# Optimization experiments

Hardware: AMD Instinct MI355X
Metric: run time of the kernel (lower is better)

The kernel has to match this reference:

```python
import jax, jax.numpy as jnp
import numpy as np

N_STATE = 64   # S4 state size N
L_MAX = 4096   # sequence length
H = 256        # number of SSM channels (d_model)
BATCH = 16


def _green_roots(Lambda, P, B, C, step, L):
    """Frequency-domain S4 kernel at the L roots of unity (Q = P, DPLR).
    Lambda,P,B,C: complex[N]; step: scalar. Returns complex[L]."""
    Omega = jnp.exp(-2j * jnp.pi * (jnp.arange(L) / L))          # (L,)
    g = (2.0 / step) * ((1.0 - Omega) / (1.0 + Omega))           # (L,)
    c = 2.0 / (1.0 + Omega)                                      # (L,)
    # four Cauchy numerators stacked: k00,k01,k10,k11
    vs = jnp.stack([C.conj() * B, C.conj() * P,
                    P.conj() * B, P.conj() * P])                 # (4,N)
    denom = g[:, None] - Lambda[None, :]                         # (L,N)
    k = jnp.einsum('kn,ln->kl', vs, 1.0 / denom)                 # (4,L)
    k00, k01, k10, k11 = k
    return c * (k00 - k01 * (1.0 / (1.0 + k11)) * k10)           # (L,)


def _kernel_freq(Lambda_re, Lambda_im, P_re, P_im, B_re, B_im,
                 C_re, C_im, log_step, L):
    Lambda = (Lambda_re + 1j * Lambda_im).astype(jnp.complex64)  # (H,N)
    P = (P_re + 1j * P_im).astype(jnp.complex64)
    Bm = (B_re + 1j * B_im).astype(jnp.complex64)
    Cm = (C_re + 1j * C_im).astype(jnp.complex64)
    step = jnp.exp(log_step)                                     # (H,)
    f = lambda lam, p, b, c, s: _green_roots(lam, p, b, c, s, L)
    return jax.vmap(f)(Lambda, P, Bm, Cm, step)                  # (H,L)


def setup_inputs() -> dict:
    key = jax.random.key(0)
    ks = jax.random.split(key, 10)
    u = jax.random.normal(ks[0], (BATCH, H, L_MAX), dtype=jnp.float32)
    # stable continuous-time poles: negative real part, spread imag parts
    Lambda_re = -0.5 * jnp.ones((H, N_STATE), jnp.float32) \
        - jax.random.uniform(ks[1], (H, N_STATE), dtype=jnp.float32)
    Lambda_im = jnp.pi * jax.random.normal(ks[2], (H, N_STATE), dtype=jnp.float32) * N_STATE / 8
    scale = 1.0 / np.sqrt(N_STATE)
    P_re = scale * jax.random.normal(ks[3], (H, N_STATE), dtype=jnp.float32)
    P_im = scale * jax.random.normal(ks[4], (H, N_STATE), dtype=jnp.float32)
    B_re = scale * jax.random.normal(ks[5], (H, N_STATE), dtype=jnp.float32)
    B_im = scale * jax.random.normal(ks[6], (H, N_STATE), dtype=jnp.float32)
    C_re = scale * jax.random.normal(ks[7], (H, N_STATE), dtype=jnp.float32)
    C_im = scale * jax.random.normal(ks[8], (H, N_STATE), dtype=jnp.float32)
    # log-uniform step in [1e-3, 1e-1] (log_step_initializer)
    log_step = (jax.random.uniform(ks[9], (H,), dtype=jnp.float32)
                * (np.log(0.1) - np.log(0.001)) + np.log(0.001)).astype(jnp.float32)
    return {"u": u, "Lambda_re": Lambda_re, "Lambda_im": Lambda_im,
            "P_re": P_re, "P_im": P_im, "B_re": B_re, "B_im": B_im,
            "C_re": C_re, "C_im": C_im, "log_step": log_step}


def reference(u, Lambda_re, Lambda_im, P_re, P_im, B_re, B_im,
              C_re, C_im, log_step):
    L = u.shape[-1]
    Kf = _kernel_freq(Lambda_re, Lambda_im, P_re, P_im, B_re, B_im,
                      C_re, C_im, log_step, L)                   # (H,L) complex
    # circular_convolution_complex, batched over (BATCH,H)
    ud = jnp.fft.fft(u, axis=-1)                                  # (B,H,L)
    y = jnp.fft.ifft(ud * Kf[None, :, :], n=L, axis=-1)
    return y.real.astype(jnp.float32)                             # (B,H,L)
```

## Files before the change

### kernel.cpp

```cpp
#include <hip/hip_runtime.h>
#include <math.h>

#define NSTATE 64
#define LEN    4096
#define NH     256
#define NB     16

__device__ float2 g_knat[NH * LEN];
__device__ float2 g_ksym[NH * LEN];
__device__ float4 g_pA[NH * NSTATE];
__device__ float4 g_pB[NH * NSTATE];
__device__ float2 g_pC[NH * NSTATE];

__device__ __forceinline__ int rev8_12(int p) {
  return ((p & 7) << 9) | (((p >> 3) & 7) << 6) | (((p >> 6) & 7) << 3) | (p >> 9);
}

__device__ __forceinline__ float2 cadd(float2 a, float2 b){ return make_float2(a.x+b.x, a.y+b.y); }
__device__ __forceinline__ float2 csub(float2 a, float2 b){ return make_float2(a.x-b.x, a.y-b.y); }
__device__ __forceinline__ float2 cmul(float2 a, float2 b){ return make_float2(a.x*b.x - a.y*b.y, a.x*b.y + a.y*b.x); }
__device__ __forceinline__ float2 mulnegi(float2 a){ return make_float2(a.y, -a.x); }
__device__ __forceinline__ float2 mulposi(float2 a){ return make_float2(-a.y, a.x); }

#define RSQ2 0.70710678118654752f

__device__ __forceinline__ void bfly8_fwd(float2 v[8]) {
  float2 a0 = cadd(v[0], v[4]), b0 = csub(v[0], v[4]);
  float2 a1 = cadd(v[1], v[5]), d1 = csub(v[1], v[5]);
  float2 a2 = cadd(v[2], v[6]), d2 = csub(v[2], v[6]);
  float2 a3 = cadd(v[3], v[7]), d3 = csub(v[3], v[7]);
  float2 b1 = make_float2(RSQ2 * (d1.x + d1.y), RSQ2 * (d1.y - d1.x));
  float2 b2 = mulnegi(d2);
  float2 b3 = make_float2(RSQ2 * (d3.y - d3.x), -RSQ2 * (d3.x + d3.y));
  float2 u0 = cadd(a0, a2), u1 = csub(a0, a2), u2 = cadd(a1, a3), u3 = csub(a1, a3);
  v[0] = cadd(u0, u2);
  v[2] = cadd(u1, mulnegi(u3));
  v[4] = csub(u0, u2);
  v[6] = cadd(u1, mulposi(u3));
  float2 w0 = cadd(b0, b2), w1 = csub(b0, b2), w2 = cadd(b1, b3), w3 = csub(b1, b3);
  v[1] = cadd(w0, w2);
  v[3] = cadd(w1, mulnegi(w3));
  v[5] = csub(w0, w2);
  v[7] = cadd(w1, mulposi(w3));
}

__device__ __forceinline__ void bfly8_inv(float2 v[8]) {
  float2 a0 = cadd(v[0], v[4]), b0 = csub(v[0], v[4]);
  float2 a1 = cadd(v[1], v[5]), d1 = csub(v[1], v[5]);
  float2 a2 = cadd(v[2], v[6]), d2 = csub(v[2], v[6]);
  float2 a3 = cadd(v[3], v[7]), d3 = csub(v[3], v[7]);
  float2 b1 = make_float2(RSQ2 * (d1.x - d1.y), RSQ2 * (d1.x + d1.y));
  float2 b2 = mulposi(d2);
  float2 b3 = make_float2(-RSQ2 * (d3.x + d3.y), RSQ2 * (d3.x - d3.y));
  float2 u0 = cadd(a0, a2), u1 = csub(a0, a2), u2 = cadd(a1, a3), u3 = csub(a1, a3);
  v[0] = cadd(u0, u2);
  v[2] = cadd(u1, mulposi(u3));
  v[4] = csub(u0, u2);
  v[6] = cadd(u1, mulnegi(u3));
  float2 w0 = cadd(b0, b2), w1 = csub(b0, b2), w2 = cadd(b1, b3), w3 = csub(b1, b3);
  v[1] = cadd(w0, w2);
  v[3] = cadd(w1, mulposi(w3));
  v[5] = csub(w0, w2);
  v[7] = cadd(w1, mulnegi(w3));
}

__device__ __forceinline__ void twiddle7(float2 v[8], float wr, float wi) {
  float2 w1 = make_float2(wr, wi);
  float2 w2 = cmul(w1, w1);
  float2 w3 = cmul(w2, w1);
  float2 w4 = cmul(w2, w2);
  float2 w5 = cmul(w3, w2);
  float2 w6 = cmul(w3, w3);
  float2 w7 = cmul(w4, w3);
  v[1] = cmul(v[1], w1); v[2] = cmul(v[2], w2); v[3] = cmul(v[3], w3);
  v[4] = cmul(v[4], w4); v[5] = cmul(v[5], w5); v[6] = cmul(v[6], w6);
  v[7] = cmul(v[7], w7);
}

__global__ __launch_bounds__(256) void s4_prep(
    const float* __restrict__ Lre, const float* __restrict__ Lim,
    const float* __restrict__ Pre, const float* __restrict__ Pim,
    const float* __restrict__ Bre, const float* __restrict__ Bim,
    const float* __restrict__ Cre, const float* __restrict__ Cim)
{
  int idx = blockIdx.x * 256 + threadIdx.x;
  if (idx >= NH * NSTATE) return;
  float lr = Lre[idx], li = Lim[idx];
  float pr = Pre[idx], pi = Pim[idx];
  float br = Bre[idx], bi = Bim[idx];
  float cr = Cre[idx], ci = Cim[idx];
  g_pA[idx] = make_float4(lr, li, pr * pr + pi * pi, 0.0f);
  g_pB[idx] = make_float4(cr * br + ci * bi, cr * bi - ci * br,
                          cr * pr + ci * pi, cr * pi - ci * pr);
  g_pC[idx] = make_float2(pr * br + pi * bi, pr * bi - pi * br);
}

__global__ __launch_bounds__(256) void s4_kernel_freq(const float* __restrict__ log_step)
{
  const int b = blockIdx.x;
  const int h = b >> 2;
  const int q = ((b & 3) << 8) | threadIdx.x;
  const float step = expf(log_step[h]);
  const float ts = 2.0f / step;
  const float NEG2PI = -6.2831853071795864769f;

  float gar, gai, car, cai, gbr, gbi, cbr, cbi;
  float gcr, gci, ccr, cci, gdr, gdi, cdr, cdi;
  {
    float so, co;
    sincosf(NEG2PI * ((float)q * (1.0f / (float)LEN)), &so, &co);
    float dr = 1.0f + co, di = so;
    float inv = 1.0f / fmaf(dr, dr, di * di);
    car = 2.0f * dr * inv; cai = -2.0f * di * inv;
    float nr = 1.0f - co, ni = -so;
    gar = ts * (fmaf(nr, dr, ni * di) * inv);
    gai = ts * (fmaf(ni, dr, -nr * di) * inv);
  }
  if (q == 0) {
    float so, co;
    sincosf(NEG2PI * 0.5f, &so, &co);
    float dr = 1.0f + co, di = so;
    float inv = 1.0f / fmaf(dr, dr, di * di);
    cbr = 2.0f * dr * inv; cbi = -2.0f * di * inv;
    float nr = 1.0f - co, ni = -so;
    gbr = ts * (fmaf(nr, dr, ni * di) * inv);
    gbi = ts * (fmaf(ni, dr, -nr * di) * inv);
  } else {
    gbr = gar; gbi = -gai; cbr = car; cbi = -cai;
  }
  {
    float so, co;
    sincosf(NEG2PI * ((float)(q + 1024) * (1.0f / (float)LEN)), &so, &co);
    float dr = 1.0f + co, di = so;
    float inv = 1.0f / fmaf(dr, dr, di * di);
    ccr = 2.0f * dr * inv; cci = -2.0f * di * inv;
    float nr = 1.0f - co, ni = -so;
    gcr = ts * (fmaf(nr, dr, ni * di) * inv);
    gci = ts * (fmaf(ni, dr, -nr * di) * inv);
  }
  gdr = gcr; gdi = -gci; cdr = ccr; cdi = -cci;

  float A00r=0,A00i=0,A01r=0,A01i=0,A10r=0,A10i=0,A11r=0,A11i=0;
  float B00r=0,B00i=0,B01r=0,B01i=0,B10r=0,B10i=0,B11r=0,B11i=0;
  float C00r=0,C00i=0,C01r=0,C01i=0,C10r=0,C10i=0,C11r=0,C11i=0;
  float D00r=0,D00i=0,D01r=0,D01i=0,D10r=0,D10i=0,D11r=0,D11i=0;

  const float4* __restrict__ pa = g_pA + h * NSTATE;
  const float4* __restrict__ pb = g_pB + h * NSTATE;
  const float2* __restrict__ pc = g_pC + h * NSTATE;

#define CAUCHY(gre, gim, k00r,k00i,k01r,k01i,k10r,k10i,k11r,k11i)            \
  {                                                                          \
    float rd = gre - Av.x, id = gim - Av.y;                                  \
    float idn = __builtin_amdgcn_rcpf(fmaf(rd, rd, id * id));                \
    float ir = rd * idn, ii = -(id * idn);                                   \
    k00r = fmaf(Bv.x, ir, k00r); k00r = fmaf(-Bv.y, ii, k00r);               \
    k00i = fmaf(Bv.x, ii, k00i); k00i = fmaf(Bv.y, ir, k00i);                \
    k01r = fmaf(Bv.z, ir, k01r); k01r = fmaf(-Bv.w, ii, k01r);               \
    k01i = fmaf(Bv.z, ii, k01i); k01i = fmaf(Bv.w, ir, k01i);                \
    k10r = fmaf(Cv.x, ir, k10r); k10r = fmaf(-Cv.y, ii, k10r);               \
    k10i = fmaf(Cv.x, ii, k10i); k10i = fmaf(Cv.y, ir, k10i);                \
    k11r = fmaf(Av.z, ir, k11r); k11i = fmaf(Av.z, ii, k11i);                \
  }

#pragma unroll 4
  for (int n = 0; n < NSTATE; ++n) {
    float4 Av = pa[n];
    float4 Bv = pb[n];
    float2 Cv = pc[n];
    CAUCHY(gar, gai, A00r,A00i,A01r,A01i,A10r,A10i,A11r,A11i)
    CAUCHY(gbr, gbi, B00r,B00i,B01r,B01i,B10r,B10i,B11r,B11i)
    CAUCHY(gcr, gci, C00r,C00i,C01r,C01i,C10r,C10i,C11r,C11i)
    CAUCHY(gdr, gdi, D00r,D00i,D01r,D01i,D10r,D10i,D11r,D11i)
  }
#undef CAUCHY

#define FINISH(cr_, ci_, k00r,k00i,k01r,k01i,k10r,k10i,k11r,k11i, Kr, Ki)    \
  {                                                                          \
    float rr = 1.0f + k11r, ri = k11i;                                       \
    float rinv = 1.0f / fmaf(rr, rr, ri * ri);                               \
    float pr_ = k01r * k10r - k01i * k10i;                                   \
    float pi_ = k01r * k10i + k01i * k10r;                                   \
    float wr = (pr_ * rr + pi_ * ri) * rinv;                                 \
    float wi = (pi_ * rr - pr_ * ri) * rinv;                                 \
    float sr = k00r - wr, si = k00i - wi;                                    \
    Kr = cr_ * sr - ci_ * si; Ki = cr_ * si + ci_ * sr;                      \
  }

  float Kar, Kai, Kbr, Kbi, Kcr, Kci, Kdr, Kdi;
  FINISH(car, cai, A00r,A00i,A01r,A01i,A10r,A10i,A11r,A11i, Kar, Kai)
  FINISH(cbr, cbi, B00r,B00i,B01r,B01i,B10r,B10i,B11r,B11i, Kbr, Kbi)
  FINISH(ccr, cci, C00r,C00i,C01r,C01i,C10r,C10i,C11r,C11i, Kcr, Kci)
  FINISH(cdr, cdi, D00r,D00i,D01r,D01i,D10r,D10i,D11r,D11i, Kdr, Kdi)
#undef FINISH

  float2* out = g_knat + (size_t)h * LEN;
  if (q == 0) {
    out[0]    = make_float2(Kar, 0.0f);
    out[2048] = make_float2(Kbr, 0.0f);
  } else {
    float fr = 0.5f * (Kar + Kbr), fi = 0.5f * (Kai - Kbi);
    out[q]        = make_float2(fr, fi);
    out[LEN - q]  = make_float2(fr, -fi);
  }
  {
    float fr = 0.5f * (Kcr + Kdr), fi = 0.5f * (Kci - Kdi);
    out[1024 + q] = make_float2(fr, fi);
    out[3072 - q] = make_float2(fr, -fi);
  }
}

__global__ __launch_bounds__(256) void s4_reorder()
{
  __shared__ float2 s[LEN];
  const int h = blockIdx.x, t = threadIdx.x;
  const float2* __restrict__ in = g_knat + (size_t)h * LEN;
  float2* __restrict__ out = g_ksym + (size_t)h * LEN;
  for (int i = t; i < LEN; i += 256) s[i ^ ((i >> 6) & 63)] = in[i];
  __syncthreads();
  for (int p = t; p < LEN; p += 256) {
    int l = rev8_12(p);
    out[p] = s[l ^ ((l >> 6) & 63)];
  }
}

__global__ __launch_bounds__(512) void s4_fftconv(const float* __restrict__ u,
                                                 float* __restrict__ y)
{
  __shared__ float2 X[4608];

  const int t = threadIdx.x;
  const int bid = blockIdx.x;
  const int h  = bid & (NH - 1);
  const int bp = bid >> 8;

  float c1, s1, c2, s2, c3, s3;
  sincosf((float)t         * (-6.2831853071795864769f / 4096.0f), &s1, &c1);
  sincosf((float)(t & 63)  * (-6.2831853071795864769f /  512.0f), &s2, &c2);
  sincosf((float)(t & 7)   * (-6.2831853071795864769f /   64.0f), &s3, &c3);

  const float* u1 = u + ((size_t)bp * NH + h) * LEN;
  const float* u2 = u + ((size_t)(bp + 8) * NH + h) * LEN;

  float2 v[8];
#pragma unroll
  for (int m = 0; m < 8; ++m)
    v[m] = make_float2(u1[t + 512 * m], u2[t + 512 * m]);
  bfly8_fwd(v);
  twiddle7(v, c1, s1);
#pragma unroll
  for (int m = 0; m < 8; ++m) X[t + 512 * m] = v[m];
  __syncthreads();

  {
    int B = t >> 6, j = t & 63, base = B * 512 + j;
#pragma unroll
    for (int m = 0; m < 8; ++m) v[m] = X[base + 64 * m];
  }
  __syncthreads();
  bfly8_fwd(v);
  twiddle7(v, c2, s2);
  {
    int B = t >> 6, j = t & 63;
#pragma unroll
    for (int m = 0; m < 8; ++m) X[68 * (8 * B + m) + j] = v[m];
  }
  __syncthreads();

  {
    int b = t >> 3, j = t & 7;
#pragma unroll
    for (int m = 0; m < 8; ++m) v[m] = X[68 * b + j + 8 * m];
  }
  __syncthreads();
  bfly8_fwd(v);
  twiddle7(v, c3, s3);
  {
    int b = t >> 3, j = t & 7;
#pragma unroll
    for (int m = 0; m < 8; ++m) X[9 * (8 * b + m) + j] = v[m];
  }
  __syncthreads();

  {
    const float4* kp = (const float4*)(g_ksym + (size_t)h * LEN + 8 * t);
    float4 k0 = kp[0], k1 = kp[1], k2 = kp[2], k3 = kp[3];
#pragma unroll
    for (int m = 0; m < 8; ++m) v[m] = X[9 * t + m];
    bfly8_fwd(v);
    v[0] = cmul(v[0], make_float2(k0.x, k0.y));
    v[1] = cmul(v[1], make_float2(k0.z, k0.w));
    v[2] = cmul(v[2], make_float2(k1.x, k1.y));
    v[3] = cmul(v[3], make_float2(k1.z, k1.w));
    v[4] = cmul(v[4], make_float2(k2.x, k2.y));
    v[5] = cmul(v[5], make_float2(k2.z, k2.w));
    v[6] = cmul(v[6], make_float2(k3.x, k3.y));
    v[7] = cmul(v[7], make_float2(k3.z, k3.w));
    bfly8_inv(v);
#pragma unroll
    for (int p = 0; p < 8; ++p) X[9 * t + p] = v[p];
  }
  __syncthreads();

  {
    int b = t >> 3, j = t & 7;
#pragma unroll
    for (int m = 0; m < 8; ++m) v[m] = X[9 * (8 * b + m) + j];
  }
  twiddle7(v, c3, -s3);
  bfly8_inv(v);
  __syncthreads();
  {
    int b = t >> 3, j = t & 7;
#pragma unroll
    for (int p = 0; p < 8; ++p) X[68 * b + j + 8 * p] = v[p];
  }
  __syncthreads();

  {
    int B = t >> 6, j = t & 63;
#pragma unroll
    for (int m = 0; m < 8; ++m) v[m] = X[68 * (8 * B + m) + j];
  }
  twiddle7(v, c2, -s2);
  bfly8_inv(v);
  __syncthreads();
  {
    int B = t >> 6, j = t & 63, base = B * 512 + j;
#pragma unroll
    for (int p = 0; p < 8; ++p) X[base + 64 * p] = v[p];
  }
  __syncthreads();

#pragma unroll
  for (int m = 0; m < 8; ++m) v[m] = X[t + 512 * m];
  twiddle7(v, c1, -s1);
  bfly8_inv(v);

  float* y1 = y + ((size_t)bp * NH + h) * LEN;
  float* y2 = y + ((size_t)(bp + 8) * NH + h) * LEN;
  const float sc = 1.0f / (float)LEN;
#pragma unroll
  for (int p = 0; p < 8; ++p) {
    y1[t + 512 * p] = v[p].x * sc;
    y2[t + 512 * p] = v[p].y * sc;
  }
}

extern "C" void kernel_launch(void* const* d_in, const int* in_sizes, int n_in,
                              void* d_out, int out_size, void* d_ws, size_t ws_size,
                              hipStream_t stream) {
  const float* u    = (const float*)d_in[0];
  const float* Lre  = (const float*)d_in[1];
  const float* Lim  = (const float*)d_in[2];
  const float* Pre  = (const float*)d_in[3];
  const float* Pim  = (const float*)d_in[4];
  const float* Bre  = (const float*)d_in[5];
  const float* Bim  = (const float*)d_in[6];
  const float* Cre  = (const float*)d_in[7];
  const float* Cim  = (const float*)d_in[8];
  const float* lstep = (const float*)d_in[9];
  float* y = (float*)d_out;

  s4_prep<<<(NH * NSTATE + 255) / 256, 256, 0, stream>>>(Lre, Lim, Pre, Pim, Bre, Bim, Cre, Cim);
  s4_kernel_freq<<<NH * 4, 256, 0, stream>>>(lstep);
  s4_reorder<<<NH, 256, 0, stream>>>();
  s4_fftconv<<<NH * (NB / 2), 512, 0, stream>>>(u, y);
}
```

Before: 187.5 us.

## Keep middle FFT stages wave-local and scatter kernel directly in bit-reversed order

Changes the shared-memory layout of the 4096-point FFT so that the middle radix-8 stages run within a single 64-lane wavefront. Those stages now use a per-wave LDS wait instead of block-wide barriers, leaving only two __syncthreads. The frequency-kernel stage also writes its output straight into the bit-reversed order, which removes the separate reorder kernel and its extra global buffer. The risk is correctness: it relies on wavefront lockstep plus lgkmcnt waits for LDS ordering, and the scattered global writes in kernel_freq are uncoalesced.

```diff
diff --git a/kernel.cpp b/kernel.cpp
--- a/kernel.cpp
+++ b/kernel.cpp
@@ -6,7 +6,6 @@
 #define NH     256
 #define NB     16
 
-__device__ float2 g_knat[NH * LEN];
 __device__ float2 g_ksym[NH * LEN];
 __device__ float4 g_pA[NH * NSTATE];
 __device__ float4 g_pB[NH * NSTATE];
@@ -77,6 +76,8 @@
   v[7] = cmul(v[7], w7);
 }
 
+#define WAVE_SYNC() asm volatile("s_waitcnt lgkmcnt(0)" ::: "memory")
+
 __global__ __launch_bounds__(256) void s4_prep(
     const float* __restrict__ Lre, const float* __restrict__ Lim,
     const float* __restrict__ Pre, const float* __restrict__ Pim,
@@ -194,33 +195,19 @@
   FINISH(cdr, cdi, D00r,D00i,D01r,D01i,D10r,D10i,D11r,D11i, Kdr, Kdi)
 #undef FINISH
 
-  float2* out = g_knat + (size_t)h * LEN;
+  float2* out = g_ksym + (size_t)h * LEN;
   if (q == 0) {
-    out[0]    = make_float2(Kar, 0.0f);
-    out[2048] = make_float2(Kbr, 0.0f);
+    out[rev8_12(0)]    = make_float2(Kar, 0.0f);
+    out[rev8_12(2048)] = make_float2(Kbr, 0.0f);
   } else {
     float fr = 0.5f * (Kar + Kbr), fi = 0.5f * (Kai - Kbi);
-    out[q]        = make_float2(fr, fi);
-    out[LEN - q]  = make_float2(fr, -fi);
+    out[rev8_12(q)]       = make_float2(fr, fi);
+    out[rev8_12(LEN - q)] = make_float2(fr, -fi);
   }
   {
     float fr = 0.5f * (Kcr + Kdr), fi = 0.5f * (Kci - Kdi);
-    out[1024 + q] = make_float2(fr, fi);
-    out[3072 - q] = make_float2(fr, -fi);
-  }
-}
-
-__global__ __launch_bounds__(256) void s4_reorder()
-{
-  __shared__ float2 s[LEN];
-  const int h = blockIdx.x, t = threadIdx.x;
-  const float2* __restrict__ in = g_knat + (size_t)h * LEN;
-  float2* __restrict__ out = g_ksym + (size_t)h * LEN;
-  for (int i = t; i < LEN; i += 256) s[i ^ ((i >> 6) & 63)] = in[i];
-  __syncthreads();
-  for (int p = t; p < LEN; p += 256) {
-    int l = rev8_12(p);
-    out[p] = s[l ^ ((l >> 6) & 63)];
+    out[rev8_12(1024 + q)] = make_float2(fr, fi);
+    out[rev8_12(3072 - q)] = make_float2(fr, -fi);
   }
 }
 
@@ -234,10 +221,16 @@
   const int h  = bid & (NH - 1);
   const int bp = bid >> 8;
 
+  const int w  = t >> 6;
+  const int i  = t & 63;
+  const int i3 = i >> 3;
+  const int i7 = i & 7;
+  const int R  = 576 * w;
+
   float c1, s1, c2, s2, c3, s3;
-  sincosf((float)t         * (-6.2831853071795864769f / 4096.0f), &s1, &c1);
-  sincosf((float)(t & 63)  * (-6.2831853071795864769f /  512.0f), &s2, &c2);
-  sincosf((float)(t & 7)   * (-6.2831853071795864769f /   64.0f), &s3, &c3);
+  sincosf((float)t  * (-6.2831853071795864769f / 4096.0f), &s1, &c1);
+  sincosf((float)i  * (-6.2831853071795864769f /  512.0f), &s2, &c2);
+  sincosf((float)i7 * (-6.2831853071795864769f /   64.0f), &s3, &c3);
 
   const float* u1 = u + ((size_t)bp * NH + h) * LEN;
   const float* u2 = u + ((size_t)(bp + 8) * NH + h) * LEN;
@@ -249,44 +242,30 @@
   bfly8_fwd(v);
   twiddle7(v, c1, s1);
 #pragma unroll
-  for (int m = 0; m < 8; ++m) X[t + 512 * m] = v[m];
+  for (int m = 0; m < 8; ++m) X[576 * m + t] = v[m];
   __syncthreads();
 
-  {
-    int B = t >> 6, j = t & 63, base = B * 512 + j;
-#pragma unroll
-    for (int m = 0; m < 8; ++m) v[m] = X[base + 64 * m];
-  }
-  __syncthreads();
+#pragma unroll
+  for (int m = 0; m < 8; ++m) v[m] = X[R + i + 64 * m];
   bfly8_fwd(v);
   twiddle7(v, c2, s2);
-  {
-    int B = t >> 6, j = t & 63;
-#pragma unroll
-    for (int m = 0; m < 8; ++m) X[68 * (8 * B + m) + j] = v[m];
-  }
-  __syncthreads();
-
-  {
-    int b = t >> 3, j = t & 7;
-#pragma unroll
-    for (int m = 0; m < 8; ++m) v[m] = X[68 * b + j + 8 * m];
-  }
-  __syncthreads();
+#pragma unroll
+  for (int m = 0; m < 8; ++m) X[R + 68 * m + i] = v[m];
+  WAVE_SYNC();
+
+#pragma unroll
+  for (int m = 0; m < 8; ++m) v[m] = X[R + 68 * i3 + i7 + 8 * m];
   bfly8_fwd(v);
   twiddle7(v, c3, s3);
-  {
-    int b = t >> 3, j = t & 7;
-#pragma unroll
-    for (int m = 0; m < 8; ++m) X[9 * (8 * b + m) + j] = v[m];
-  }
-  __syncthreads();
+#pragma unroll
+  for (int m = 0; m < 8; ++m) X[R + 9 * (8 * i3 + m) + i7] = v[m];
+  WAVE_SYNC();
 
   {
     const float4* kp = (const float4*)(g_ksym + (size_t)h * LEN + 8 * t);
     float4 k0 = kp[0], k1 = kp[1], k2 = kp[2], k3 = kp[3];
 #pragma unroll
-    for (int m = 0; m < 8; ++m) v[m] = X[9 * t + m];
+    for (int m = 0; m < 8; ++m) v[m] = X[R + 9 * i + m];
     bfly8_fwd(v);
     v[0] = cmul(v[0], make_float2(k0.x, k0.y));
     v[1] = cmul(v[1], make_float2(k0.z, k0.w));
@@ -298,42 +277,28 @@
     v[7] = cmul(v[7], make_float2(k3.z, k3.w));
     bfly8_inv(v);
 #pragma unroll
-    for (int p = 0; p < 8; ++p) X[9 * t + p] = v[p];
-  }
-  __syncthreads();
-
-  {
-    int b = t >> 3, j = t & 7;
-#pragma unroll
-    for (int m = 0; m < 8; ++m) v[m] = X[9 * (8 * b + m) + j];
-  }
+    for (int p = 0; p < 8; ++p) X[R + 9 * i + p] = v[p];
+  }
+  WAVE_SYNC();
+
+#pragma unroll
+  for (int m = 0; m < 8; ++m) v[m] = X[R + 9 * (8 * i3 + m) + i7];
   twiddle7(v, c3, -s3);
   bfly8_inv(v);
-  __syncthreads();
-  {
-    int b = t >> 3, j = t & 7;
-#pragma unroll
-    for (int p = 0; p < 8; ++p) X[68 * b + j + 8 * p] = v[p];
-  }
-  __syncthreads();
-
-  {
-    int B = t >> 6, j = t & 63;
-#pragma unroll
-    for (int m = 0; m < 8; ++m) v[m] = X[68 * (8 * B + m) + j];
-  }
+#pragma unroll
+  for (int p = 0; p < 8; ++p) X[R + 68 * i3 + i7 + 8 * p] = v[p];
+  WAVE_SYNC();
+
+#pragma unroll
+  for (int m = 0; m < 8; ++m) v[m] = X[R + 68 * m + i];
   twiddle7(v, c2, -s2);
   bfly8_inv(v);
+#pragma unroll
+  for (int p = 0; p < 8; ++p) X[R + i + 64 * p] = v[p];
   __syncthreads();
-  {
-    int B = t >> 6, j = t & 63, base = B * 512 + j;
-#pragma unroll
-    for (int p = 0; p < 8; ++p) X[base + 64 * p] = v[p];
-  }
-  __syncthreads();
-
-#pragma unroll
-  for (int m = 0; m < 8; ++m) v[m] = X[t + 512 * m];
+
+#pragma unroll
+  for (int m = 0; m < 8; ++m) v[m] = X[576 * m + t];
   twiddle7(v, c1, -s1);
   bfly8_inv(v);
 
@@ -364,6 +329,5 @@
 
   s4_prep<<<(NH * NSTATE + 255) / 256, 256, 0, stream>>>(Lre, Lim, Pre, Pim, Bre, Bim, Cre, Cim);
   s4_kernel_freq<<<NH * 4, 256, 0, stream>>>(lstep);
-  s4_reorder<<<NH, 256, 0, stream>>>();
   s4_fftconv<<<NH * (NB / 2), 512, 0, stream>>>(u, y);
 }
```

Measured after the change: 180.4 us. 3.8% less time.
